# Kernel optimization log

Measured on AMD Instinct MI355X. Metric: run time of the kernel, lower is better.

Reference implementation:

```python
import jax, jax.numpy as jnp
import numpy as np
from jax import lax

N_EXPERTS = 8


def setup_inputs() -> dict:
    key = jax.random.key(0)
    ks = jax.random.split(key, 5)
    B, F, H, C, E = 32768, 512, 256, 100, N_EXPERTS
    x = jax.random.normal(ks[0], (B, F), dtype=jnp.float32)
    W1 = jax.random.normal(ks[1], (E, F, H), dtype=jnp.float32) * (1.0 / np.sqrt(F))
    b1 = jnp.zeros((E, H), dtype=jnp.float32)
    W2 = jax.random.normal(ks[2], (E, H, C), dtype=jnp.float32) * (1.0 / np.sqrt(H))
    b2 = jnp.zeros((E, C), dtype=jnp.float32)
    Wg = jax.random.normal(ks[3], (F, E), dtype=jnp.float32) * (1.0 / np.sqrt(F))
    return {"x": x, "W1": W1, "b1": b1, "W2": W2, "b2": b2, "Wg": Wg, "k": 2}


def reference(x, W1, b1, W2, b2, Wg, k):
    B = x.shape[0]
    # experts: per-expert 2-layer MLP, vectorized over the expert dim e
    h = jax.nn.relu(jnp.einsum('bf,efh->ebh', x, W1) + b1[:, None, :])  # [E,B,H]
    preds = jnp.einsum('ebh,ehc->ebc', h, W2) + b2[:, None, :]          # [E,B,C]
    # fixed gating: softmax over gate logits, top-k, hard 1/k weights
    probs = jax.nn.softmax(x @ Wg, axis=-1)                             # [B,E]
    _, top_idx = lax.top_k(probs, k)                                    # [B,k]
    weights = jnp.zeros_like(probs).at[jnp.arange(B)[:, None], top_idx].set(1.0 / k)
    # combined prediction: gate-weighted sum of per-expert softmaxed logits
    combined = jnp.einsum('ebc,be->bc', jax.nn.softmax(preds, axis=-1), weights)
    part_sizes = (weights > 0).sum(axis=0)  # samples routed per expert
    return combined, preds, part_sizes
```

## Files before the change

kernel.cpp:

```cpp
#include <hip/hip_runtime.h>
#include <hip/hip_bf16.h>
#include <math.h>

#define B_ 32768
#define F_ 512
#define H_ 256
#define C_ 100
#define CP 112
#define E_ 8

typedef __attribute__((ext_vector_type(8))) short bf16x8;
typedef __attribute__((ext_vector_type(4))) float f32x4;

__device__ __forceinline__ unsigned short f2b(float f) {
    unsigned int u = __float_as_uint(f);
    return (unsigned short)((u + 0x7fffu + ((u >> 16) & 1u)) >> 16);
}

__device__ __forceinline__ void gll16(const void* g, void* l) {
    __builtin_amdgcn_global_load_lds((__attribute__((address_space(1))) void*)(g),
                                     (__attribute__((address_space(3))) void*)(l),
                                     16, 0, 0);
}

__global__ __launch_bounds__(256) void k0_cvt_x(const float* __restrict__ x,
                                                unsigned short* __restrict__ xb) {
    size_t t = (size_t)blockIdx.x * 256 + threadIdx.x;
    #pragma unroll
    for (int it = 0; it < 4; ++it) {
        size_t i4 = t + (size_t)it * (4096 * 256);
        float4 v = ((const float4*)x)[i4];
        ushort4 o;
        o.x = f2b(v.x); o.y = f2b(v.y); o.z = f2b(v.z); o.w = f2b(v.w);
        ((ushort4*)xb)[i4] = o;
    }
}

__global__ __launch_bounds__(256) void k0_tr_w1(const float* __restrict__ W1,
                                                unsigned short* __restrict__ w1t) {
    __shared__ float tile[32][33];
    int e = blockIdx.z, fb = blockIdx.x * 32, hb = blockIdx.y * 32;
    int tx = threadIdx.x, ty = threadIdx.y;
    #pragma unroll
    for (int j = 0; j < 4; ++j)
        tile[ty + 8 * j][tx] = W1[((size_t)(e * F_ + fb + ty + 8 * j)) * H_ + hb + tx];
    __syncthreads();
    #pragma unroll
    for (int j = 0; j < 4; ++j)
        w1t[((size_t)(e * H_ + hb + ty + 8 * j)) * F_ + fb + tx] = f2b(tile[tx][ty + 8 * j]);
}

__global__ __launch_bounds__(256) void k0_cvt_w2(const float* __restrict__ W2,
                                                 unsigned short* __restrict__ w2t) {
    int idx = blockIdx.x * 256 + threadIdx.x;
    if (idx >= E_ * CP * H_) return;
    int e = idx / (CP * H_);
    int r = idx - e * (CP * H_);
    int c = r / H_, h = r - c * H_;
    float v = (c < C_) ? W2[((size_t)(e * H_ + h)) * C_ + c] : 0.0f;
    w2t[idx] = f2b(v);
}

__global__ __launch_bounds__(256) void k1_gate(const float* __restrict__ x,
                                               const float* __restrict__ Wg,
                                               int* __restrict__ routes,
                                               float* __restrict__ part) {
    __shared__ float sWg[F_ * E_];
    __shared__ int cnt[E_];
    int tid = threadIdx.x;
    for (int i = tid; i < F_ * E_; i += 256) sWg[i] = Wg[i];
    if (tid < E_) cnt[tid] = 0;
    __syncthreads();

    int r = tid >> 3, eidx = tid & 7;
    int row = blockIdx.x * 32 + r;
    const float* xr = x + (size_t)row * F_;
    double acc = 0.0;
    for (int f = 0; f < F_; f += 4) {
        float4 xv = *(const float4*)(xr + f);
        acc += (double)xv.x * (double)sWg[(f + 0) * 8 + eidx];
        acc += (double)xv.y * (double)sWg[(f + 1) * 8 + eidx];
        acc += (double)xv.z * (double)sWg[(f + 2) * 8 + eidx];
        acc += (double)xv.w * (double)sWg[(f + 3) * 8 + eidx];
    }
    double v = acc; int ie = eidx;
    #pragma unroll
    for (int off = 1; off < 8; off <<= 1) {
        double ov = __shfl_xor(v, off);
        int oi = __shfl_xor(ie, off);
        if (ov > v || (ov == v && oi < ie)) { v = ov; ie = oi; }
    }
    int e1 = ie;
    double v2 = (eidx == e1) ? -1e300 : acc; int ie2 = eidx;
    #pragma unroll
    for (int off = 1; off < 8; off <<= 1) {
        double ov = __shfl_xor(v2, off);
        int oi = __shfl_xor(ie2, off);
        if (ov > v2 || (ov == v2 && oi < ie2)) { v2 = ov; ie2 = oi; }
    }
    int e2 = ie2;
    if (eidx == 0) {
        routes[row] = e1 | (e2 << 3);
        atomicAdd(&cnt[e1], 1);
        atomicAdd(&cnt[e2], 1);
    }
    __syncthreads();
    if (tid < E_) atomicAdd(&part[tid], (float)cnt[tid]);
}

__global__ __launch_bounds__(256) void k2_moe(const unsigned short* __restrict__ xbf,
                                              const unsigned short* __restrict__ w1t,
                                              const unsigned short* __restrict__ w2t,
                                              const float* __restrict__ b1,
                                              const float* __restrict__ b2,
                                              float* __restrict__ preds) {
    __shared__ __align__(16) char smem[54272];
    const int tid = threadIdx.x;
    const int w = tid >> 6, lane = tid & 63;
    const int q = lane >> 4, ln = lane & 15;
    const int e = blockIdx.y;
    const int rowBase = blockIdx.x * 64;

    const int jsw = (lane & 3) ^ ((lane >> 3) & 3);
    const int ra = w * 16 + (lane >> 2);
    const unsigned short* srcA = xbf + (size_t)(rowBase + ra) * F_ + 8 * jsw;
    const unsigned short* srcB0 = w1t + (size_t)(e * H_ + (w * 64 + 0  + (lane >> 2))) * F_ + 8 * jsw;
    const unsigned short* srcB1 = w1t + (size_t)(e * H_ + (w * 64 + 16 + (lane >> 2))) * F_ + 8 * jsw;
    const unsigned short* srcB2 = w1t + (size_t)(e * H_ + (w * 64 + 32 + (lane >> 2))) * F_ + 8 * jsw;
    const unsigned short* srcB3 = w1t + (size_t)(e * H_ + (w * 64 + 48 + (lane >> 2))) * F_ + 8 * jsw;
    char* dstA = smem + w * 1024;
    char* dstB0 = smem + 4096 + (w * 64 + 0)  * 64;
    char* dstB1 = smem + 4096 + (w * 64 + 16) * 64;
    char* dstB2 = smem + 4096 + (w * 64 + 32) * 64;
    char* dstB3 = smem + 4096 + (w * 64 + 48) * 64;

    const int jp = q ^ ((ln >> 1) & 3);
    int offA[4], offB[4];
    #pragma unroll
    for (int mt = 0; mt < 4; ++mt) offA[mt] = ((mt * 16 + ln) * 4 + jp) * 16;
    #pragma unroll
    for (int nt = 0; nt < 4; ++nt) offB[nt] = 4096 + ((w * 64 + nt * 16 + ln) * 4 + jp) * 16;

    f32x4 acc[4][4];
    #pragma unroll
    for (int i = 0; i < 4; ++i)
        #pragma unroll
        for (int j = 0; j < 4; ++j) acc[i][j] = (f32x4){0.f, 0.f, 0.f, 0.f};

    for (int kk = 0; kk < 16; ++kk) {
        gll16(srcA, dstA);
        gll16(srcB0, dstB0);
        gll16(srcB1, dstB1);
        gll16(srcB2, dstB2);
        gll16(srcB3, dstB3);
        srcA += 32; srcB0 += 32; srcB1 += 32; srcB2 += 32; srcB3 += 32;
        __syncthreads();
        bf16x8 af[4], bfr[4];
        #pragma unroll
        for (int mt = 0; mt < 4; ++mt) af[mt] = *(const bf16x8*)(smem + offA[mt]);
        #pragma unroll
        for (int nt = 0; nt < 4; ++nt) bfr[nt] = *(const bf16x8*)(smem + offB[nt]);
        #pragma unroll
        for (int mt = 0; mt < 4; ++mt)
            #pragma unroll
            for (int nt = 0; nt < 4; ++nt)
                acc[mt][nt] = __builtin_amdgcn_mfma_f32_16x16x32_bf16(af[mt], bfr[nt], acc[mt][nt], 0, 0, 0);
        __syncthreads();
    }

    float bias1[4];
    #pragma unroll
    for (int nt = 0; nt < 4; ++nt) bias1[nt] = b1[e * H_ + w * 64 + nt * 16 + ln];
    #pragma unroll
    for (int mt = 0; mt < 4; ++mt)
        #pragma unroll
        for (int nt = 0; nt < 4; ++nt)
            #pragma unroll
            for (int r2 = 0; r2 < 4; ++r2) {
                int rr = mt * 16 + q * 4 + r2;
                int col = w * 64 + nt * 16 + ln;
                float v = fmaxf(acc[mt][nt][r2] + bias1[nt], 0.0f);
                *(unsigned short*)(smem + 20480 + rr * 528 + col * 2) = f2b(v);
            }

    f32x4 acc2[7];
    #pragma unroll
    for (int i = 0; i < 7; ++i) acc2[i] = (f32x4){0.f, 0.f, 0.f, 0.f};
    const int offH = 20480 + (w * 16 + ln) * 528 + q * 16;
    unsigned int* sw2 = (unsigned int*)smem;
    const unsigned int* w2d = (const unsigned int*)w2t;
    for (int kc = 0; kc < 8; ++kc) {
        __syncthreads();
        for (int idx = tid; idx < CP * 16; idx += 256) {
            int n = idx >> 4, kd = idx & 15;
            sw2[n * 20 + kd] = w2d[(e * CP + n) * 128 + kc * 16 + kd];
        }
        __syncthreads();
        bf16x8 hb = *(const bf16x8*)(smem + offH + kc * 64);
        #pragma unroll
        for (int mt = 0; mt < 7; ++mt) {
            bf16x8 a = *(const bf16x8*)(smem + (mt * 16 + ln) * 80 + q * 16);
            acc2[mt] = __builtin_amdgcn_mfma_f32_16x16x32_bf16(a, hb, acc2[mt], 0, 0, 0);
        }
    }

    int row = rowBase + w * 16 + ln;
    #pragma unroll
    for (int mt = 0; mt < 7; ++mt) {
        int c0 = mt * 16 + q * 4;
        if (c0 + 3 < C_) {
            f32x4 bias = *(const f32x4*)(b2 + e * C_ + c0);
            f32x4 o = acc2[mt] + bias;
            *(f32x4*)(preds + ((size_t)e * B_ + row) * C_ + c0) = o;
        }
    }
}

__global__ __launch_bounds__(256) void k3_combine(const float* __restrict__ preds,
                                                  const int* __restrict__ routes,
                                                  float* __restrict__ combined) {
    __shared__ float pbuf[4][104];
    int tid = threadIdx.x, wv = tid >> 6, lane = tid & 63;
    int row = blockIdx.x * 2 + (wv >> 1);
    int rt = routes[row];
    int e = (wv & 1) ? ((rt >> 3) & 7) : (rt & 7);
    const float* pr = preds + ((size_t)e * B_ + row) * C_;
    float a0 = (lane < C_) ? pr[lane] : -1e30f;
    float a1 = (lane + 64 < C_) ? pr[lane + 64] : -1e30f;
    float m = fmaxf(a0, a1);
    #pragma unroll
    for (int off = 32; off; off >>= 1) m = fmaxf(m, __shfl_xor(m, off));
    float s0 = (lane < C_) ? expf(a0 - m) : 0.f;
    float s1 = (lane + 64 < C_) ? expf(a1 - m) : 0.f;
    float s = s0 + s1;
    #pragma unroll
    for (int off = 32; off; off >>= 1) s += __shfl_xor(s, off);
    float inv = 0.5f / s;
    if (lane < C_) pbuf[wv][lane] = s0 * inv;
    if (lane + 64 < C_) pbuf[wv][lane + 64] = s1 * inv;
    __syncthreads();
    if (tid < C_)
        combined[(size_t)(blockIdx.x * 2) * C_ + tid] = pbuf[0][tid] + pbuf[1][tid];
    else if (tid >= 128 && tid < 128 + C_)
        combined[(size_t)(blockIdx.x * 2 + 1) * C_ + (tid - 128)] = pbuf[2][tid - 128] + pbuf[3][tid - 128];
}

extern "C" void kernel_launch(void* const* d_in, const int* in_sizes, int n_in,
                              void* d_out, int out_size, void* d_ws, size_t ws_size,
                              hipStream_t stream) {
    (void)in_sizes; (void)n_in; (void)out_size;
    const float* x  = (const float*)d_in[0];
    const float* W1 = (const float*)d_in[1];
    const float* b1 = (const float*)d_in[2];
    const float* W2 = (const float*)d_in[3];
    const float* b2 = (const float*)d_in[4];
    const float* Wg = (const float*)d_in[5];

    float* out = (float*)d_out;
    float* combined = out;
    float* preds = out + (size_t)B_ * C_;
    float* part  = out + (size_t)B_ * C_ + (size_t)E_ * B_ * C_;

    char* ws = (char*)d_ws;
    unsigned short* xbf = (unsigned short*)ws;
    unsigned short* w1t = (unsigned short*)(ws + 33554432);
    unsigned short* w2t = (unsigned short*)(ws + 35651584);
    int* routes = (int*)(ws + 36110336);
    if (ws_size < 36241408) return;

    hipMemsetAsync(part, 0, E_ * sizeof(float), stream);
    k0_cvt_x<<<4096, 256, 0, stream>>>(x, xbf);
    k0_tr_w1<<<dim3(F_ / 32, H_ / 32, E_), dim3(32, 8), 0, stream>>>(W1, w1t);
    k0_cvt_w2<<<(E_ * CP * H_ + 255) / 256, 256, 0, stream>>>(W2, w2t);
    k1_gate<<<B_ / 32, 256, 0, stream>>>(x, Wg, routes, part);
    k2_moe<<<dim3(B_ / 64, E_), 256, 0, stream>>>(xbf, w1t, w2t, b1, b2, preds);
    k3_combine<<<B_ / 2, 256, 0, stream>>>(preds, routes, combined);
}
```

Measured before the change: 427.2 us.

## Deepen GEMM1 K-tile to 64 and stream W2 from global into registers

The first GEMM now loads a 64-wide K slice per iteration (8 iterations instead of 16) with an 8-way XOR swizzle, halving the number of barriers in the main loop. The second GEMM no longer stages W2 through shared memory with two barriers per chunk; each lane loads its W2 fragments directly from global memory into double-buffered registers. Shared memory drops from about 54KB to 40KB, which may allow more blocks per CU. The cost is higher register pressure from the 14 bf16x8 W2 registers and redundant global reads of W2 by every wave.

```diff
diff --git a/kernel.cpp b/kernel.cpp
--- a/kernel.cpp
+++ b/kernel.cpp
@@ -114,32 +114,23 @@
                                               const float* __restrict__ b1,
                                               const float* __restrict__ b2,
                                               float* __restrict__ preds) {
-    __shared__ __align__(16) char smem[54272];
+    __shared__ __align__(16) char smem[40960];
     const int tid = threadIdx.x;
     const int w = tid >> 6, lane = tid & 63;
     const int q = lane >> 4, ln = lane & 15;
     const int e = blockIdx.y;
     const int rowBase = blockIdx.x * 64;
 
-    const int jsw = (lane & 3) ^ ((lane >> 3) & 3);
-    const int ra = w * 16 + (lane >> 2);
-    const unsigned short* srcA = xbf + (size_t)(rowBase + ra) * F_ + 8 * jsw;
-    const unsigned short* srcB0 = w1t + (size_t)(e * H_ + (w * 64 + 0  + (lane >> 2))) * F_ + 8 * jsw;
-    const unsigned short* srcB1 = w1t + (size_t)(e * H_ + (w * 64 + 16 + (lane >> 2))) * F_ + 8 * jsw;
-    const unsigned short* srcB2 = w1t + (size_t)(e * H_ + (w * 64 + 32 + (lane >> 2))) * F_ + 8 * jsw;
-    const unsigned short* srcB3 = w1t + (size_t)(e * H_ + (w * 64 + 48 + (lane >> 2))) * F_ + 8 * jsw;
+    const int sub = lane >> 3;
+    const int j8 = (lane & 7) ^ sub;
+    const unsigned short* srcA0 = xbf + (size_t)(rowBase + w * 8 + sub) * F_ + 8 * j8;
+    const unsigned short* srcB0 = w1t + (size_t)(e * H_ + w * 8 + sub) * F_ + 8 * j8;
     char* dstA = smem + w * 1024;
-    char* dstB0 = smem + 4096 + (w * 64 + 0)  * 64;
-    char* dstB1 = smem + 4096 + (w * 64 + 16) * 64;
-    char* dstB2 = smem + 4096 + (w * 64 + 32) * 64;
-    char* dstB3 = smem + 4096 + (w * 64 + 48) * 64;
-
-    const int jp = q ^ ((ln >> 1) & 3);
-    int offA[4], offB[4];
-    #pragma unroll
-    for (int mt = 0; mt < 4; ++mt) offA[mt] = ((mt * 16 + ln) * 4 + jp) * 16;
-    #pragma unroll
-    for (int nt = 0; nt < 4; ++nt) offB[nt] = 4096 + ((w * 64 + nt * 16 + ln) * 4 + jp) * 16;
+    char* dstB = smem + 8192 + w * 1024;
+
+    float bias1[4];
+    #pragma unroll
+    for (int nt = 0; nt < 4; ++nt) bias1[nt] = b1[e * H_ + w * 64 + nt * 16 + ln];
 
     f32x4 acc[4][4];
     #pragma unroll
@@ -147,30 +138,33 @@
         #pragma unroll
         for (int j = 0; j < 4; ++j) acc[i][j] = (f32x4){0.f, 0.f, 0.f, 0.f};
 
-    for (int kk = 0; kk < 16; ++kk) {
-        gll16(srcA, dstA);
-        gll16(srcB0, dstB0);
-        gll16(srcB1, dstB1);
-        gll16(srcB2, dstB2);
-        gll16(srcB3, dstB3);
-        srcA += 32; srcB0 += 32; srcB1 += 32; srcB2 += 32; srcB3 += 32;
+    for (int kk = 0; kk < 8; ++kk) {
+        const int ko = kk * 64;
+        gll16(srcA0 + ko, dstA);
+        gll16(srcA0 + 32 * F_ + ko, dstA + 4096);
+        #pragma unroll
+        for (int i = 0; i < 8; ++i)
+            gll16(srcB0 + (size_t)i * 32 * F_ + ko, dstB + i * 4096);
         __syncthreads();
-        bf16x8 af[4], bfr[4];
-        #pragma unroll
-        for (int mt = 0; mt < 4; ++mt) af[mt] = *(const bf16x8*)(smem + offA[mt]);
-        #pragma unroll
-        for (int nt = 0; nt < 4; ++nt) bfr[nt] = *(const bf16x8*)(smem + offB[nt]);
-        #pragma unroll
-        for (int mt = 0; mt < 4; ++mt)
+        #pragma unroll
+        for (int ks = 0; ks < 2; ++ks) {
+            const int slot = ((ks * 4 + q) ^ (ln & 7)) * 16;
+            bf16x8 af[4], bfr[4];
+            #pragma unroll
+            for (int mt = 0; mt < 4; ++mt)
+                af[mt] = *(const bf16x8*)(smem + (mt * 16 + ln) * 128 + slot);
             #pragma unroll
             for (int nt = 0; nt < 4; ++nt)
-                acc[mt][nt] = __builtin_amdgcn_mfma_f32_16x16x32_bf16(af[mt], bfr[nt], acc[mt][nt], 0, 0, 0);
+                bfr[nt] = *(const bf16x8*)(smem + 8192 + (w * 64 + nt * 16 + ln) * 128 + slot);
+            #pragma unroll
+            for (int mt = 0; mt < 4; ++mt)
+                #pragma unroll
+                for (int nt = 0; nt < 4; ++nt)
+                    acc[mt][nt] = __builtin_amdgcn_mfma_f32_16x16x32_bf16(af[mt], bfr[nt], acc[mt][nt], 0, 0, 0);
+        }
         __syncthreads();
     }
 
-    float bias1[4];
-    #pragma unroll
-    for (int nt = 0; nt < 4; ++nt) bias1[nt] = b1[e * H_ + w * 64 + nt * 16 + ln];
     #pragma unroll
     for (int mt = 0; mt < 4; ++mt)
         #pragma unroll
@@ -180,28 +174,34 @@
                 int rr = mt * 16 + q * 4 + r2;
                 int col = w * 64 + nt * 16 + ln;
                 float v = fmaxf(acc[mt][nt][r2] + bias1[nt], 0.0f);
-                *(unsigned short*)(smem + 20480 + rr * 528 + col * 2) = f2b(v);
+                *(unsigned short*)(smem + rr * 528 + col * 2) = f2b(v);
             }
 
+    const unsigned short* w2base = w2t + ((size_t)e * CP + ln) * H_ + q * 8;
+    bf16x8 wreg[2][7];
+    #pragma unroll
+    for (int mt = 0; mt < 7; ++mt)
+        wreg[0][mt] = *(const bf16x8*)(w2base + mt * 16 * H_);
+
     f32x4 acc2[7];
     #pragma unroll
     for (int i = 0; i < 7; ++i) acc2[i] = (f32x4){0.f, 0.f, 0.f, 0.f};
-    const int offH = 20480 + (w * 16 + ln) * 528 + q * 16;
-    unsigned int* sw2 = (unsigned int*)smem;
-    const unsigned int* w2d = (const unsigned int*)w2t;
+    const int offH = (w * 16 + ln) * 528 + q * 16;
+
+    __syncthreads();
+
+    #pragma unroll
     for (int kc = 0; kc < 8; ++kc) {
-        __syncthreads();
-        for (int idx = tid; idx < CP * 16; idx += 256) {
-            int n = idx >> 4, kd = idx & 15;
-            sw2[n * 20 + kd] = w2d[(e * CP + n) * 128 + kc * 16 + kd];
+        const int cur = kc & 1, nxt = cur ^ 1;
+        if (kc < 7) {
+            #pragma unroll
+            for (int mt = 0; mt < 7; ++mt)
+                wreg[nxt][mt] = *(const bf16x8*)(w2base + mt * 16 * H_ + (kc + 1) * 32);
         }
-        __syncthreads();
         bf16x8 hb = *(const bf16x8*)(smem + offH + kc * 64);
         #pragma unroll
-        for (int mt = 0; mt < 7; ++mt) {
-            bf16x8 a = *(const bf16x8*)(smem + (mt * 16 + ln) * 80 + q * 16);
-            acc2[mt] = __builtin_amdgcn_mfma_f32_16x16x32_bf16(a, hb, acc2[mt], 0, 0, 0);
-        }
+        for (int mt = 0; mt < 7; ++mt)
+            acc2[mt] = __builtin_amdgcn_mfma_f32_16x16x32_bf16(wreg[cur][mt], hb, acc2[mt], 0, 0, 0);
     }
 
     int row = rowBase + w * 16 + ln;
```

After: 421.4 us. Within noise of the previous version (-1.4%).
